# Performance work log

Measured on AMD Instinct MI355X. Metric: run time of the kernel, lower is better.

Reference implementation:

```python
import jax, jax.numpy as jnp
import numpy as np

D, N = 512, 128

def setup_inputs() -> dict:
    key = jax.random.key(0)
    k1, k2 = jax.random.split(key)
    A = jax.random.normal(k1, (D, D), dtype=jnp.float32)
    Q, _ = jnp.linalg.qr(A)                      # orthonormal orbitals (reortho_orbitals QR)
    P = Q[:, :N].astype(jnp.float32)             # D x N Slater orbitals
    positions = jnp.sort(jax.random.choice(k2, D, shape=(N,), replace=False)).astype(jnp.int32)
    return {"P": P, "positions": positions}


def _lu_pivots(A):
    """Diagonal of U from unpivoted Gaussian elimination.
    Leading principal minors of A are cumulative products of these pivots."""
    Dn = A.shape[-1]
    idx = jnp.arange(Dn)
    def step(M, j):
        pivot = M[j, j]
        col = jnp.where(idx > j, M[:, j] / pivot, 0.0)   # elimination multipliers
        M = M - col[:, None] * M[j][None, :]             # rank-1 update (memory bound)
        return M, pivot
    _, piv = jax.lax.scan(step, A, idx)
    return piv


def _cond_probs(P, positions):
    dtype = P.dtype
    G = jnp.eye(D, dtype=dtype) - P @ P.T                 # D x D
    onehots = jax.nn.one_hot(positions, D, dtype=dtype)   # [N, D]
    occ_prefix = jnp.cumsum(onehots, axis=0) - onehots    # occ of sites chosen before step k
    # A_k = G - diag(occ_prefix[k]): denominator/base matrix of step k
    A = G[None, :, :] - occ_prefix[:, :, None] * jnp.eye(D, dtype=dtype)[None]
    piv = jax.vmap(_lu_pivots)(A)                         # [N, D] pivots u_jj
    k = jnp.arange(N)
    xmin = jnp.where(k == 0, 0, positions[jnp.maximum(k - 1, 0)] + 1)  # [N]
    xmax = D - N + k + 1
    i = jnp.arange(D)[None, :]
    # probs[k,i] = -(det Gnum)/(det Gdenom) = (1 - u_ii) * prod_{j=xmin..i-1} u_jj
    q = jnp.where(i >= xmin[:, None], piv, jnp.ones((), dtype))
    c = jnp.concatenate([jnp.ones((N, 1), dtype), jnp.cumprod(q, axis=1)[:, :-1]], axis=1)
    probs = c * (1.0 - piv)
    valid = (i >= xmin[:, None]) & (i < xmax[:, None])
    probs = jnp.where(valid, probs, 0.0)
    probs = jnp.where(jnp.abs(probs) > 1e-15, probs, 0.0)  # torch.where(|p|>1e-15, p, 0)
    return probs


def reference(P, positions):
    probs = _cond_probs(P, positions)                     # [N, D] conditional distributions
    picked = jnp.take_along_axis(probs, positions[:, None], axis=1)[:, 0]
    log_prob_sample = jnp.sum(jnp.log(picked))            # log of prob_sample (product underflows)
    return probs, log_prob_sample
```

## Files before the change

kernel.cpp:

```cpp
#include <hip/hip_runtime.h>
#include <math.h>

#define DD 512
#define NN 128
#define XBASE 385

#define OFF_M      0
#define OFF_LP     262144
#define OFF_UP     278528
#define OFF_CPIV   294912
#define OFF_SHAD   295424
#define OFF_SSNAP  295552
#define OFF_FPIV   297600
#define OFF_LOG    363136
#define OFF_MI     363264
#define OFF_POSMAP 364032
#define OFF_MISC   364544
#define OFF_FORK   364608

template<bool RECALL>
__device__ __forceinline__ float w0_block_lu(float (&a)[32], float sh,
    unsigned long long shmask, int elim, int recl,
    float* __restrict__ pvsL, float (*dblkL)[36], float (*dblkTL)[36],
    float* __restrict__ recp, int gbase, int gmin, int lane)
{
    bool mine = (shmask >> lane) & 1ull;
#pragma unroll
    for (int j = 0; j < 32; ++j) {
        if (j > recl) break;
        float d  = __shfl(a[j], j);
        float sj = __shfl(sh, j);
        if (lane == 0) {
            int g = gbase + j;
            if (RECALL || g > gmin) recp[g] = d;
        }
        if (j >= elim) break;
        float pv = ((shmask >> j) & 1ull) ? sj : d;
        if (lane == 0) pvsL[j] = pv;
        bool below = lane > j;
        if (below) a[j] = a[j] / pv;
        float m = a[j];
#pragma unroll
        for (int c = j + 1; c < 32; ++c) {
            float bj = __shfl(a[c], j);
            if (below) {
                a[c] = fmaf(-m, bj, a[c]);
                if (mine && lane == c) sh = fmaf(-m, bj, sh);
            }
        }
    }
#pragma unroll
    for (int c = 0; c < 32; ++c) { dblkL[lane][c] = a[c]; dblkTL[c][lane] = a[c]; }
    return sh;
}

__device__ __forceinline__ void solve_L21_row(float (&a)[32], const float (*dblk)[36],
                                              const float* __restrict__ pvs) {
#pragma unroll
    for (int c = 0; c < 32; ++c) {
        a[c] = a[c] / pvs[c];
        float m = a[c];
        int j = c + 1;
#pragma unroll
        for (; (j & 3) && j < 32; ++j) a[j] = fmaf(-m, dblk[c][j], a[j]);
#pragma unroll
        for (; j + 3 < 32; j += 4) {
            const float4 u = *(const float4*)&dblk[c][j];
            a[j+0] = fmaf(-m, u.x, a[j+0]); a[j+1] = fmaf(-m, u.y, a[j+1]);
            a[j+2] = fmaf(-m, u.z, a[j+2]); a[j+3] = fmaf(-m, u.w, a[j+3]);
        }
    }
}

__device__ __forceinline__ void solve_U12_col(float (&v)[32], const float (*dblkT)[36]) {
#pragma unroll
    for (int c = 0; c < 31; ++c) {
        float vc = v[c];
        int j = c + 1;
#pragma unroll
        for (; (j & 3) && j < 32; ++j) v[j] = fmaf(-dblkT[c][j], vc, v[j]);
#pragma unroll
        for (; j + 3 < 32; j += 4) {
            const float4 u = *(const float4*)&dblkT[c][j];
            v[j+0] = fmaf(-u.x, vc, v[j+0]); v[j+1] = fmaf(-u.y, vc, v[j+1]);
            v[j+2] = fmaf(-u.z, vc, v[j+2]); v[j+3] = fmaf(-u.w, vc, v[j+3]);
        }
    }
}

__global__ void k_build(const float* __restrict__ P, float* __restrict__ ws) {
    __shared__ float Pr[32][129];
    __shared__ float Pc[32][129];
    int r0 = blockIdx.x * 32, c0 = blockIdx.y * 32, tid = threadIdx.x;
    for (int idx = tid; idx < 32 * 128; idx += 256) {
        int r = idx >> 7, t = idx & 127;
        Pr[r][t] = P[(r0 + r) * NN + t];
        Pc[r][t] = P[(c0 + r) * NN + t];
    }
    __syncthreads();
    int cl = tid & 31, rl0 = tid >> 5;
    for (int e = 0; e < 4; ++e) {
        int rl = rl0 + e * 8;
        float acc = 0.0f;
#pragma unroll 8
        for (int t = 0; t < 128; ++t) acc = fmaf(Pr[rl][t], Pc[cl][t], acc);
        int gr = r0 + rl, gc = c0 + cl;
        ws[OFF_M + gr * DD + gc] = ((gr == gc) ? 1.0f : 0.0f) - acc;
    }
}

__global__ void k_meta(const int* __restrict__ pos, float* __restrict__ ws) {
    int* mi   = (int*)ws + OFF_MI;
    int* pm   = (int*)ws + OFF_POSMAP;
    int* misc = (int*)ws + OFF_MISC;
    __shared__ int sS[128];
    int k = threadIdx.x;
    int p = pos[k];
    mi[k] = p;
    mi[128 + k] = (k == 0) ? 0 : (pos[k - 1] + 1);
    int x = XBASE + k;
    mi[256 + k] = x;
    int j0 = (p >> 5) << 5;
    mi[384 + k] = j0;
    int s = x - j0;
    mi[512 + k] = s;
    sS[k] = s * s;
    float g = ws[OFF_M + p * DD + p];
    ws[OFF_SHAD + k]  = g - 1.0f;
    ws[OFF_SSNAP + k] = g - 1.0f;
    for (int i = k; i < 512; i += 128) pm[i] = -1;
    __syncthreads();
    pm[p] = k;
    if (k == 0) {
        int acc = 0;
        for (int i = 0; i < 128; ++i) { mi[640 + i] = acc; acc += sS[i]; }
        misc[0] = pos[127];
    }
}

__global__ void k_snap0(float* __restrict__ ws) {
    const int* mi = (const int*)ws + OFF_MI;
    int r0 = blockIdx.x * 32, c0 = blockIdx.y * 32, tid = threadIdx.x;
    int cl = tid & 31, rl0 = tid >> 5;
    for (int k = 0; k < 128; ++k) {
        if (mi[384 + k] != 0) continue;
        int x = mi[256 + k];
        if (r0 >= x || c0 >= x) continue;
        int s = mi[512 + k];
        float* buf = ws + OFF_FORK + mi[640 + k];
        for (int e = 0; e < 4; ++e) {
            int gr = r0 + rl0 + e * 8, gc = c0 + cl;
            if (gr < x && gc < x) buf[gr * s + gc] = ws[OFF_M + gr * DD + gc];
        }
    }
}

__global__ void __launch_bounds__(1024) k_panel(float* __restrict__ ws, int t) {
    const int* misc = (const int*)ws + OFF_MISC;
    int j0 = t * 32;
    if (j0 > misc[0]) return;
    const int* pm = (const int*)ws + OFF_POSMAP;
    __shared__ float dblk[32][36], dblkT[32][36];
    __shared__ float pvs[32];
    __shared__ float shadL[128];
    __shared__ int   chfL[32];
    int tid = threadIdx.x;
    int jn = j0 + 32, w = DD - jn;
    if (tid < 128) { float sv = ws[OFF_SHAD + tid]; shadL[tid] = sv; ws[OFF_SSNAP + t * 128 + tid] = sv; }
    if (tid < 32) chfL[tid] = pm[j0 + tid];
    __syncthreads();
    if (tid < 32) {
        float a[32];
#pragma unroll
        for (int c = 0; c < 32; ++c) a[c] = ws[OFF_M + (size_t)(j0 + tid) * DD + j0 + c];
        int cf = chfL[tid];
        float sh = (cf >= 0) ? shadL[cf] : 0.0f;
        unsigned long long bm = __ballot(cf >= 0);
        sh = w0_block_lu<true>(a, sh, bm, 32, 31, pvs, dblk, dblkT, ws + OFF_CPIV, j0, -1, tid);
        if (cf >= 0) ws[OFF_SHAD + cf] = sh;
    }
    __syncthreads();
    for (int task = tid; task < 2 * w; task += 1024) {
        if (task < w) {
            int r = jn + task;
            const float* src = ws + OFF_M + (size_t)r * DD + j0;
            float a[32];
#pragma unroll
            for (int c = 0; c < 32; ++c) a[c] = src[c];
            solve_L21_row(a, dblk, pvs);
            float* dst = ws + OFF_LP + (size_t)r * 32;
#pragma unroll
            for (int c = 0; c < 32; ++c) dst[c] = a[c];
        } else {
            int col = jn + (task - w);
            float v[32];
#pragma unroll
            for (int j = 0; j < 32; ++j) v[j] = ws[OFF_M + (size_t)(j0 + j) * DD + col];
            solve_U12_col(v, dblkT);
#pragma unroll
            for (int j = 0; j < 32; ++j) ws[OFF_UP + j * DD + col] = v[j];
        }
    }
}

__global__ void k_trail(float* __restrict__ ws, int t) {
    const int* misc = (const int*)ws + OFF_MISC;
    int j0 = t * 32, jn = j0 + 32;
    if (jn > misc[0]) return;
    const int* mi = (const int*)ws + OFF_MI;
    const int* pm = (const int*)ws + OFF_POSMAP;
    int r0 = blockIdx.x * 32, c0 = blockIdx.y * 32, tid = threadIdx.x;
    if (r0 < jn || c0 < jn) return;
    __shared__ float Lt[32][36], Ut[32][36];
    int cl = tid & 31, rl0 = tid >> 5;
    for (int e = 0; e < 4; ++e) {
        int rl = rl0 + e * 8;
        Lt[rl][cl] = ws[OFF_LP + (r0 + rl) * 32 + cl];
        Ut[rl][cl] = ws[OFF_UP + rl * DD + c0 + cl];
    }
    __syncthreads();
    int r = tid >> 3, c4 = (tid & 7) << 2;
    int gr = r0 + r;
    float acc[4];
#pragma unroll
    for (int j = 0; j < 4; ++j) acc[j] = ws[OFF_M + (size_t)gr * DD + c0 + c4 + j];
#pragma unroll 8
    for (int jj = 0; jj < 32; ++jj) {
        float lv = Lt[r][jj];
        const float4 uv = *(const float4*)&Ut[jj][c4];
        acc[0] = fmaf(-lv, uv.x, acc[0]); acc[1] = fmaf(-lv, uv.y, acc[1]);
        acc[2] = fmaf(-lv, uv.z, acc[2]); acc[3] = fmaf(-lv, uv.w, acc[3]);
    }
    if (r0 == c0 && r >= c4 && r < c4 + 4) {
        int kk = pm[gr];
        if (kk >= 0) {
            float sv = ws[OFF_SHAD + kk];
#pragma unroll 8
            for (int jj = 0; jj < 32; ++jj) sv = fmaf(-Lt[r][jj], Ut[jj][r], sv);
            ws[OFF_SHAD + kk] = sv;
        }
    }
#pragma unroll
    for (int j = 0; j < 4; ++j) ws[OFF_M + (size_t)gr * DD + c0 + c4 + j] = acc[j];
    for (int k = 0; k < 128; ++k) {
        if (mi[384 + k] != jn) continue;
        int x = mi[256 + k];
        if (r0 >= x || c0 >= x || gr >= x) continue;
        int s = mi[512 + k];
        float* buf = ws + OFF_FORK + mi[640 + k];
#pragma unroll
        for (int j = 0; j < 4; ++j) {
            int gc = c0 + c4 + j;
            if (gc < x) buf[(size_t)(gr - jn) * s + (gc - jn)] = acc[j];
        }
    }
}

__global__ void __launch_bounds__(1024) k_fork(float* __restrict__ ws) {
    const int* mi = (const int*)ws + OFF_MI;
    const int* pm = (const int*)ws + OFF_POSMAP;
    int k = blockIdx.x;
    int p = mi[k], x = mi[256 + k], j0 = mi[384 + k], s = mi[512 + k];
    if (p >= x - 1) return;
    float* buf = ws + OFF_FORK + mi[640 + k];
    float* fpv = ws + OFF_FPIV + k * DD;
    int tstage = j0 >> 5;
    __shared__ float dblk[32][36], dblkT[32][36];
    __shared__ float pvs[32];
    __shared__ float fpanT[32][360];
    __shared__ float fstrip[32][360];
    int tid = threadIdx.x;
    int xl = s - 1;
    for (int pf0 = 0;; pf0 += 32) {
        int rem = xl - pf0;
        if (tid < 32) {
            float a[32];
#pragma unroll
            for (int c = 0; c < 32; ++c) {
                int rr = pf0 + tid, cc = pf0 + c;
                a[c] = (rr <= xl && cc <= xl) ? buf[(size_t)rr * s + cc] : 0.0f;
            }
            float sh = 0.0f;
            unsigned long long bm = 0ull;
            if (pf0 == 0) {
                int g = j0 + tid;
                int kk = pm[g];
                bool ch = (kk >= 0 && g < p);
                if (ch) sh = ws[OFF_SSNAP + tstage * 128 + kk];
                bm = __ballot(ch);
            }
            int elim = rem < 32 ? rem : 32;
            int recl = rem < 31 ? rem : 31;
            w0_block_lu<false>(a, sh, bm, elim, recl, pvs, dblk, dblkT, fpv, j0 + pf0, p, tid);
        }
        if (rem < 32) break;
        __syncthreads();
        int tw = s - pf0 - 32;
        if (tid < tw) {
            int r = pf0 + 32 + tid;
            const float* src = buf + (size_t)r * s + pf0;
            float a[32];
#pragma unroll
            for (int c = 0; c < 32; ++c) a[c] = src[c];
            solve_L21_row(a, dblk, pvs);
#pragma unroll
            for (int c = 0; c < 32; ++c) fpanT[c][tid] = a[c];
        } else if (tid >= 512 && tid < 512 + tw) {
            int u = tid - 512;
            int col = pf0 + 32 + u;
            float v[32];
#pragma unroll
            for (int j = 0; j < 32; ++j) v[j] = buf[(size_t)(pf0 + j) * s + col];
            solve_U12_col(v, dblkT);
#pragma unroll
            for (int j = 0; j < 32; ++j) fstrip[j][u] = v[j];
        }
        __syncthreads();
        {
            int ntr = (tw + 7) >> 3;
            int nt2 = ntr * ntr;
            for (int tile = tid; tile < nt2; tile += 1024) {
                int ti = tile / ntr;
                int tr = ti << 3, tc = (tile - ti * ntr) << 3;
                int rb = pf0 + 32 + tr, cb = pf0 + 32 + tc;
                if (tr + 8 <= tw && tc + 8 <= tw) {
                    float acc[8][8];
#pragma unroll
                    for (int i = 0; i < 8; ++i)
#pragma unroll
                        for (int j = 0; j < 8; ++j) acc[i][j] = buf[(size_t)(rb + i) * s + cb + j];
#pragma unroll 2
                    for (int jj = 0; jj < 32; ++jj) {
                        const float4 a0 = *(const float4*)&fpanT[jj][tr];
                        const float4 a1 = *(const float4*)&fpanT[jj][tr + 4];
                        const float4 b0 = *(const float4*)&fstrip[jj][tc];
                        const float4 b1 = *(const float4*)&fstrip[jj][tc + 4];
                        float av[8] = {a0.x, a0.y, a0.z, a0.w, a1.x, a1.y, a1.z, a1.w};
                        float bv[8] = {b0.x, b0.y, b0.z, b0.w, b1.x, b1.y, b1.z, b1.w};
#pragma unroll
                        for (int i = 0; i < 8; ++i)
#pragma unroll
                            for (int j = 0; j < 8; ++j)
                                acc[i][j] = fmaf(-av[i], bv[j], acc[i][j]);
                    }
#pragma unroll
                    for (int i = 0; i < 8; ++i)
#pragma unroll
                        for (int j = 0; j < 8; ++j) buf[(size_t)(rb + i) * s + cb + j] = acc[i][j];
                } else {
                    int nr = tw - tr; nr = nr > 8 ? 8 : nr;
                    int nc = tw - tc; nc = nc > 8 ? 8 : nc;
                    float acc[8][8];
#pragma unroll
                    for (int i = 0; i < 8; ++i)
#pragma unroll
                        for (int j = 0; j < 8; ++j)
                            acc[i][j] = (i < nr && j < nc) ? buf[(size_t)(rb + i) * s + cb + j] : 0.0f;
                    for (int jj = 0; jj < 32; ++jj) {
                        float av[8], bv[8];
#pragma unroll
                        for (int i = 0; i < 8; ++i) av[i] = (i < nr) ? fpanT[jj][tr + i] : 0.0f;
#pragma unroll
                        for (int j = 0; j < 8; ++j) bv[j] = (j < nc) ? fstrip[jj][tc + j] : 0.0f;
#pragma unroll
                        for (int i = 0; i < 8; ++i)
#pragma unroll
                            for (int j = 0; j < 8; ++j)
                                acc[i][j] = fmaf(-av[i], bv[j], acc[i][j]);
                    }
#pragma unroll
                    for (int i = 0; i < 8; ++i)
#pragma unroll
                        for (int j = 0; j < 8; ++j)
                            if (i < nr && j < nc) buf[(size_t)(rb + i) * s + cb + j] = acc[i][j];
                }
            }
        }
        __syncthreads();
    }
}

__global__ void k_epilogue(float* __restrict__ ws, float* __restrict__ out) {
    const int* mi = (const int*)ws + OFF_MI;
    int k = blockIdx.x, tid = threadIdx.x;
    __shared__ float row[512];
    __shared__ float pivs[512];
    int c = mi[128 + k], p = mi[k], x = mi[256 + k];
    for (int i = tid; i < 512; i += 256) {
        row[i] = 0.0f;
        pivs[i] = (i <= p) ? ws[OFF_CPIV + i] : ws[OFF_FPIV + k * DD + i];
    }
    __syncthreads();
    if (tid == 0) {
        float cp = 1.0f;
        for (int i = c; i < x; ++i) {
            float pv = pivs[i];
            float pr = cp * (1.0f - pv);
            row[i] = (fabsf(pr) > 1e-15f) ? pr : 0.0f;
            cp = cp * pv;
        }
        ws[OFF_LOG + k] = logf(row[p]);
    }
    __syncthreads();
    for (int i = tid; i < 512; i += 256) out[k * DD + i] = row[i];
}

__global__ void k_logsum(float* __restrict__ ws, float* __restrict__ out) {
    __shared__ float lv[128];
    int tid = threadIdx.x;
    if (tid < 64) { lv[tid] = ws[OFF_LOG + tid]; lv[tid + 64] = ws[OFF_LOG + tid + 64]; }
    __syncthreads();
    if (tid == 0) {
        double sacc = 0.0;
        for (int i = 0; i < 128; ++i) sacc += (double)lv[i];
        out[65536] = (float)sacc;
    }
}

extern "C" void kernel_launch(void* const* d_in, const int* in_sizes, int n_in,
                              void* d_out, int out_size, void* d_ws, size_t ws_size,
                              hipStream_t stream) {
    const float* P   = (const float*)d_in[0];
    const int*   pos = (const int*)d_in[1];
    float* ws  = (float*)d_ws;
    float* out = (float*)d_out;

    k_build<<<dim3(16, 16), 256, 0, stream>>>(P, ws);
    k_meta<<<1, 128, 0, stream>>>(pos, ws);
    k_snap0<<<dim3(16, 16), 256, 0, stream>>>(ws);
    for (int t = 0; t < 16; ++t) {
        k_panel<<<1, 1024, 0, stream>>>(ws, t);
        if (t < 15) k_trail<<<dim3(16, 16), 256, 0, stream>>>(ws, t);
    }
    k_fork<<<128, 1024, 0, stream>>>(ws);
    k_epilogue<<<128, 256, 0, stream>>>(ws, out);
    k_logsum<<<1, 64, 0, stream>>>(ws, out);
}
```

Before: 2.136 ms.

## Fuse panel factorization into trailing update and retile fork GEMM per wavefront

```diff
diff --git a/kernel.cpp b/kernel.cpp
--- a/kernel.cpp
+++ b/kernel.cpp
@@ -6,8 +6,6 @@
 #define XBASE 385
 
 #define OFF_M      0
-#define OFF_LP     262144
-#define OFF_UP     278528
 #define OFF_CPIV   294912
 #define OFF_SHAD   295424
 #define OFF_SSNAP  295552
@@ -20,7 +18,7 @@
 
 template<bool RECALL>
 __device__ __forceinline__ float w0_block_lu(float (&a)[32], float sh,
-    unsigned long long shmask, int elim, int recl,
+    unsigned long long shmask, int elim, int recl, bool wrec,
     float* __restrict__ pvsL, float (*dblkL)[36], float (*dblkTL)[36],
     float* __restrict__ recp, int gbase, int gmin, int lane)
 {
@@ -30,7 +28,7 @@
         if (j > recl) break;
         float d  = __shfl(a[j], j);
         float sj = __shfl(sh, j);
-        if (lane == 0) {
+        if (lane == 0 && wrec) {
             int g = gbase + j;
             if (RECALL || g > gmin) recp[g] = d;
         }
@@ -155,68 +153,47 @@
     }
 }
 
-__global__ void __launch_bounds__(1024) k_panel(float* __restrict__ ws, int t) {
+__global__ void __launch_bounds__(256) k_stage(float* __restrict__ ws, int t) {
     const int* misc = (const int*)ws + OFF_MISC;
-    int j0 = t * 32;
+    int j0 = t * 32, jn = j0 + 32;
     if (j0 > misc[0]) return;
+    const int* mi = (const int*)ws + OFF_MI;
     const int* pm = (const int*)ws + OFF_POSMAP;
+    int bx = blockIdx.x, by = blockIdx.y;
+    bool root = (bx == 0 && by == 0);
+    bool trail = (jn <= misc[0]);
+    if (!trail && !root) return;
     __shared__ float dblk[32][36], dblkT[32][36];
     __shared__ float pvs[32];
-    __shared__ float shadL[128];
-    __shared__ int   chfL[32];
+    __shared__ float Lt[32][36], Ut[32][36];
     int tid = threadIdx.x;
-    int jn = j0 + 32, w = DD - jn;
-    if (tid < 128) { float sv = ws[OFF_SHAD + tid]; shadL[tid] = sv; ws[OFF_SSNAP + t * 128 + tid] = sv; }
-    if (tid < 32) chfL[tid] = pm[j0 + tid];
-    __syncthreads();
     if (tid < 32) {
         float a[32];
 #pragma unroll
         for (int c = 0; c < 32; ++c) a[c] = ws[OFF_M + (size_t)(j0 + tid) * DD + j0 + c];
-        int cf = chfL[tid];
-        float sh = (cf >= 0) ? shadL[cf] : 0.0f;
+        int cf = pm[j0 + tid];
+        float sh = (cf >= 0) ? ws[OFF_SSNAP + t * 128 + cf] : 0.0f;
         unsigned long long bm = __ballot(cf >= 0);
-        sh = w0_block_lu<true>(a, sh, bm, 32, 31, pvs, dblk, dblkT, ws + OFF_CPIV, j0, -1, tid);
-        if (cf >= 0) ws[OFF_SHAD + cf] = sh;
-    }
-    __syncthreads();
-    for (int task = tid; task < 2 * w; task += 1024) {
-        if (task < w) {
-            int r = jn + task;
-            const float* src = ws + OFF_M + (size_t)r * DD + j0;
-            float a[32];
-#pragma unroll
-            for (int c = 0; c < 32; ++c) a[c] = src[c];
-            solve_L21_row(a, dblk, pvs);
-            float* dst = ws + OFF_LP + (size_t)r * 32;
-#pragma unroll
-            for (int c = 0; c < 32; ++c) dst[c] = a[c];
-        } else {
-            int col = jn + (task - w);
-            float v[32];
-#pragma unroll
-            for (int j = 0; j < 32; ++j) v[j] = ws[OFF_M + (size_t)(j0 + j) * DD + col];
-            solve_U12_col(v, dblkT);
-#pragma unroll
-            for (int j = 0; j < 32; ++j) ws[OFF_UP + j * DD + col] = v[j];
-        }
-    }
-}
-
-__global__ void k_trail(float* __restrict__ ws, int t) {
-    const int* misc = (const int*)ws + OFF_MISC;
-    int j0 = t * 32, jn = j0 + 32;
-    if (jn > misc[0]) return;
-    const int* mi = (const int*)ws + OFF_MI;
-    const int* pm = (const int*)ws + OFF_POSMAP;
-    int r0 = blockIdx.x * 32, c0 = blockIdx.y * 32, tid = threadIdx.x;
-    if (r0 < jn || c0 < jn) return;
-    __shared__ float Lt[32][36], Ut[32][36];
-    int cl = tid & 31, rl0 = tid >> 5;
-    for (int e = 0; e < 4; ++e) {
-        int rl = rl0 + e * 8;
-        Lt[rl][cl] = ws[OFF_LP + (r0 + rl) * 32 + cl];
-        Ut[rl][cl] = ws[OFF_UP + rl * DD + c0 + cl];
+        w0_block_lu<true>(a, sh, bm, 32, 31, root, pvs, dblk, dblkT, ws + OFF_CPIV, j0, -1, tid);
+    }
+    if (!trail) return;
+    int r0 = jn + bx * 32, c0 = jn + by * 32;
+    __syncthreads();
+    if (tid < 32) {
+        float a[32];
+#pragma unroll
+        for (int c = 0; c < 32; ++c) a[c] = ws[OFF_M + (size_t)(r0 + tid) * DD + j0 + c];
+        solve_L21_row(a, dblk, pvs);
+#pragma unroll
+        for (int c = 0; c < 32; ++c) Lt[tid][c] = a[c];
+    } else if (tid >= 64 && tid < 96) {
+        int u = tid - 64;
+        float v[32];
+#pragma unroll
+        for (int j = 0; j < 32; ++j) v[j] = ws[OFF_M + (size_t)(j0 + j) * DD + c0 + u];
+        solve_U12_col(v, dblkT);
+#pragma unroll
+        for (int j = 0; j < 32; ++j) Ut[j][u] = v[j];
     }
     __syncthreads();
     int r = tid >> 3, c4 = (tid & 7) << 2;
@@ -231,13 +208,14 @@
         acc[0] = fmaf(-lv, uv.x, acc[0]); acc[1] = fmaf(-lv, uv.y, acc[1]);
         acc[2] = fmaf(-lv, uv.z, acc[2]); acc[3] = fmaf(-lv, uv.w, acc[3]);
     }
-    if (r0 == c0 && r >= c4 && r < c4 + 4) {
+    if (bx == by && r >= c4 && r < c4 + 4) {
         int kk = pm[gr];
         if (kk >= 0) {
             float sv = ws[OFF_SHAD + kk];
 #pragma unroll 8
             for (int jj = 0; jj < 32; ++jj) sv = fmaf(-Lt[r][jj], Ut[jj][r], sv);
             ws[OFF_SHAD + kk] = sv;
+            if (root) ws[OFF_SSNAP + (t + 1) * 128 + kk] = sv;
         }
     }
 #pragma unroll
@@ -256,7 +234,7 @@
     }
 }
 
-__global__ void __launch_bounds__(1024) k_fork(float* __restrict__ ws) {
+__global__ void __launch_bounds__(512, 2) k_fork(float* __restrict__ ws) {
     const int* mi = (const int*)ws + OFF_MI;
     const int* pm = (const int*)ws + OFF_POSMAP;
     int k = blockIdx.x;
@@ -270,6 +248,9 @@
     __shared__ float fpanT[32][360];
     __shared__ float fstrip[32][360];
     int tid = threadIdx.x;
+    int lane = tid & 63;
+    int li = lane >> 3, lj = lane & 7;
+    int wid = tid >> 6;
     int xl = s - 1;
     for (int pf0 = 0;; pf0 += 32) {
         int rem = xl - pf0;
@@ -291,39 +272,44 @@
             }
             int elim = rem < 32 ? rem : 32;
             int recl = rem < 31 ? rem : 31;
-            w0_block_lu<false>(a, sh, bm, elim, recl, pvs, dblk, dblkT, fpv, j0 + pf0, p, tid);
+            w0_block_lu<false>(a, sh, bm, elim, recl, true, pvs, dblk, dblkT, fpv, j0 + pf0, p, tid);
         }
         if (rem < 32) break;
         __syncthreads();
         int tw = s - pf0 - 32;
-        if (tid < tw) {
-            int r = pf0 + 32 + tid;
-            const float* src = buf + (size_t)r * s + pf0;
-            float a[32];
-#pragma unroll
-            for (int c = 0; c < 32; ++c) a[c] = src[c];
-            solve_L21_row(a, dblk, pvs);
-#pragma unroll
-            for (int c = 0; c < 32; ++c) fpanT[c][tid] = a[c];
-        } else if (tid >= 512 && tid < 512 + tw) {
-            int u = tid - 512;
-            int col = pf0 + 32 + u;
-            float v[32];
-#pragma unroll
-            for (int j = 0; j < 32; ++j) v[j] = buf[(size_t)(pf0 + j) * s + col];
-            solve_U12_col(v, dblkT);
-#pragma unroll
-            for (int j = 0; j < 32; ++j) fstrip[j][u] = v[j];
+        for (int task = tid; task < 2 * tw; task += 512) {
+            if (task < tw) {
+                int r = pf0 + 32 + task;
+                const float* src = buf + (size_t)r * s + pf0;
+                float a[32];
+#pragma unroll
+                for (int c = 0; c < 32; ++c) a[c] = src[c];
+                solve_L21_row(a, dblk, pvs);
+#pragma unroll
+                for (int c = 0; c < 32; ++c) fpanT[c][task] = a[c];
+            } else {
+                int u = task - tw;
+                int col = pf0 + 32 + u;
+                float v[32];
+#pragma unroll
+                for (int j = 0; j < 32; ++j) v[j] = buf[(size_t)(pf0 + j) * s + col];
+                solve_U12_col(v, dblkT);
+#pragma unroll
+                for (int j = 0; j < 32; ++j) fstrip[j][u] = v[j];
+            }
         }
         __syncthreads();
         {
-            int ntr = (tw + 7) >> 3;
-            int nt2 = ntr * ntr;
-            for (int tile = tid; tile < nt2; tile += 1024) {
-                int ti = tile / ntr;
-                int tr = ti << 3, tc = (tile - ti * ntr) << 3;
-                int rb = pf0 + 32 + tr, cb = pf0 + 32 + tc;
-                if (tr + 8 <= tw && tc + 8 <= tw) {
+            int base = pf0 + 32;
+            int nmacro = (tw + 63) >> 6;
+            int nmac2 = nmacro * nmacro;
+            for (int m = wid; m < nmac2; m += 8) {
+                int wr = m / nmacro, wc = m - wr * nmacro;
+                int tr = ((wr << 3) + li) << 3;
+                int tc = ((wc << 3) + lj) << 3;
+                int rb = base + tr, cb = base + tc;
+                bool interior = (((wr + 1) << 6) <= tw) && (((wc + 1) << 6) <= tw);
+                if (interior) {
                     float acc[8][8];
 #pragma unroll
                     for (int i = 0; i < 8; ++i)
@@ -348,31 +334,33 @@
 #pragma unroll
                         for (int j = 0; j < 8; ++j) buf[(size_t)(rb + i) * s + cb + j] = acc[i][j];
                 } else {
-                    int nr = tw - tr; nr = nr > 8 ? 8 : nr;
-                    int nc = tw - tc; nc = nc > 8 ? 8 : nc;
-                    float acc[8][8];
-#pragma unroll
-                    for (int i = 0; i < 8; ++i)
-#pragma unroll
-                        for (int j = 0; j < 8; ++j)
-                            acc[i][j] = (i < nr && j < nc) ? buf[(size_t)(rb + i) * s + cb + j] : 0.0f;
-                    for (int jj = 0; jj < 32; ++jj) {
-                        float av[8], bv[8];
-#pragma unroll
-                        for (int i = 0; i < 8; ++i) av[i] = (i < nr) ? fpanT[jj][tr + i] : 0.0f;
-#pragma unroll
-                        for (int j = 0; j < 8; ++j) bv[j] = (j < nc) ? fstrip[jj][tc + j] : 0.0f;
+                    int nr = tw - tr; nr = nr < 0 ? 0 : (nr > 8 ? 8 : nr);
+                    int nc = tw - tc; nc = nc < 0 ? 0 : (nc > 8 ? 8 : nc);
+                    if (nr > 0 && nc > 0) {
+                        float acc[8][8];
 #pragma unroll
                         for (int i = 0; i < 8; ++i)
 #pragma unroll
                             for (int j = 0; j < 8; ++j)
-                                acc[i][j] = fmaf(-av[i], bv[j], acc[i][j]);
+                                acc[i][j] = (i < nr && j < nc) ? buf[(size_t)(rb + i) * s + cb + j] : 0.0f;
+                        for (int jj = 0; jj < 32; ++jj) {
+                            float av[8], bv[8];
+#pragma unroll
+                            for (int i = 0; i < 8; ++i) av[i] = (i < nr) ? fpanT[jj][tr + i] : 0.0f;
+#pragma unroll
+                            for (int j = 0; j < 8; ++j) bv[j] = (j < nc) ? fstrip[jj][tc + j] : 0.0f;
+#pragma unroll
+                            for (int i = 0; i < 8; ++i)
+#pragma unroll
+                                for (int j = 0; j < 8; ++j)
+                                    acc[i][j] = fmaf(-av[i], bv[j], acc[i][j]);
+                        }
+#pragma unroll
+                        for (int i = 0; i < 8; ++i)
+#pragma unroll
+                            for (int j = 0; j < 8; ++j)
+                                if (i < nr && j < nc) buf[(size_t)(rb + i) * s + cb + j] = acc[i][j];
                     }
-#pragma unroll
-                    for (int i = 0; i < 8; ++i)
-#pragma unroll
-                        for (int j = 0; j < 8; ++j)
-                            if (i < nr && j < nc) buf[(size_t)(rb + i) * s + cb + j] = acc[i][j];
                 }
             }
         }
@@ -429,10 +417,10 @@
     k_meta<<<1, 128, 0, stream>>>(pos, ws);
     k_snap0<<<dim3(16, 16), 256, 0, stream>>>(ws);
     for (int t = 0; t < 16; ++t) {
-        k_panel<<<1, 1024, 0, stream>>>(ws, t);
-        if (t < 15) k_trail<<<dim3(16, 16), 256, 0, stream>>>(ws, t);
-    }
-    k_fork<<<128, 1024, 0, stream>>>(ws);
+        int gt = 15 - t; if (gt < 1) gt = 1;
+        k_stage<<<dim3(gt, gt), 256, 0, stream>>>(ws, t);
+    }
+    k_fork<<<128, 512, 0, stream>>>(ws);
     k_epilogue<<<128, 256, 0, stream>>>(ws, out);
     k_logsum<<<1, 64, 0, stream>>>(ws, out);
 }
```

Result: faster. 1.884 ms (-11.8%).
